# Optimization experiments

Hardware: AMD Instinct MI355X
Metric: run time of the kernel (lower is better)

Reference implementation:

```python
import jax, jax.numpy as jnp
import numpy as np

NX, NY = 8192, 8192
FX, FY = 1024, 1024
EMB, EMB_OUT = 512, 512


def setup_inputs() -> dict:
    key = jax.random.key(0)
    ks = jax.random.split(key, 8)
    s = lambda f: 1.0 / np.sqrt(f)
    return {
        "x": jax.random.normal(ks[0], (NX, FX), jnp.float32),
        "y": jax.random.normal(ks[1], (NY, FY), jnp.float32),
        "Wx": jax.random.uniform(ks[2], (FX, EMB), jnp.float32, -s(FX), s(FX)),
        "bx": jax.random.uniform(ks[3], (EMB,), jnp.float32, -s(FX), s(FX)),
        "Wy": jax.random.uniform(ks[4], (FY, EMB), jnp.float32, -s(FY), s(FY)),
        "by": jax.random.uniform(ks[5], (EMB,), jnp.float32, -s(FY), s(FY)),
        "Wg": jax.random.uniform(ks[6], (EMB, EMB_OUT), jnp.float32, -s(EMB), s(EMB)),
        "bg": jax.random.uniform(ks[7], (EMB_OUT,), jnp.float32, -s(EMB), s(EMB)),
    }


def reference(x, y, Wx, bx, Wy, by, Wg, bg):
    # Linear projections: [Nx, emb], [Ny, emb]
    xp = x @ Wx + bx
    yp = y @ Wy + by
    # Pairwise affinity (Dice-coefficient style normalization)
    A_ = xp @ yp.T                              # [Nx, Ny]
    Dcol = jnp.sum(xp * xp, axis=1)[:, None]    # ||x_i||^2, diag of xp@xp.T
    Drow = jnp.sum(yp * yp, axis=1)[None, :]    # ||y_j||^2, diag of yp@yp.T
    A = 2.0 * A_ / (Dcol + Drow)                # [Nx, Ny]
    # Weighted aggregation over x nodes, then ReLU MLP
    gwf = A.T @ xp                              # [Ny, emb]
    return jax.nn.relu(gwf @ Wg + bg)           # [Ny, emb_out]
```

## Files before the change

### kernel.cpp

```cpp
#include <hip/hip_runtime.h>
#include <hip/hip_bf16.h>


typedef __attribute__((ext_vector_type(8))) short bf16x8;
typedef __attribute__((ext_vector_type(4))) short bf16x4;
typedef __attribute__((ext_vector_type(4))) float f32x4;

__device__ __forceinline__ short f2b(float f) {
    unsigned int u = __builtin_bit_cast(unsigned int, f);
    unsigned int r = (u + 0x7fffu + ((u >> 16) & 1u)) >> 16;
    return (short)r;
}
__device__ __forceinline__ float b2f(short s) {
    unsigned int u = ((unsigned int)(unsigned short)s) << 16;
    return __builtin_bit_cast(float, u);
}

__device__ __forceinline__ void cp16(const void* g, void* l) {
    __builtin_amdgcn_global_load_lds(
        (const __attribute__((address_space(1))) void*)g,
        (__attribute__((address_space(3))) void*)l, 16, 0, 0);
}

constexpr int EPI_XP = 0;
constexpr int EPI_BF = 1;
constexpr int EPI_AT = 2;

template<int EPI, int TM, int TN>
__device__ __forceinline__ void gemm_core(
    const short* __restrict__ A, int lda,
    const short* __restrict__ Bt, int ldb,
    int N, int K, int bm, int bn, int kbase,
    const float* __restrict__ bias,
    short* __restrict__ outb,
    float* __restrict__ Dacc,
    const float* __restrict__ Drow, const float* __restrict__ Dcol)
{
    constexpr int FRM = (TN == 128) ? (TM / 32) : 2;
    __shared__ __align__(16) short As[TM * 32];
    __shared__ __align__(16) short Bs[TN * 32];

    const int tid  = threadIdx.x;
    const int wave = tid >> 6;
    const int lane = tid & 63;
    const int quad = lane >> 4;
    const int l15  = lane & 15;
    const int wn   = (TN == 128) ? (wave & 1) * 64 : 0;
    const int wm   = (TN == 128) ? (wave >> 1) * (FRM * 16) : wave * 32;

    f32x4 acc[FRM][4];
#pragma unroll
    for (int i = 0; i < FRM; i++)
#pragma unroll
        for (int j = 0; j < 4; j++) acc[i][j] = f32x4{0.f, 0.f, 0.f, 0.f};

    for (int k0 = kbase; k0 < kbase + K; k0 += 32) {
#pragma unroll
        for (int s = 0; s < TM / 64; s++) {
            const int seg = tid + 256 * s;
            const int row = seg >> 2, c8 = seg & 3;
            cp16(&A[(size_t)(bm + row) * lda + k0 + c8 * 8], &As[seg * 8]);
        }
#pragma unroll
        for (int s = 0; s < TN / 64; s++) {
            const int seg = tid + 256 * s;
            const int row = seg >> 2, c8 = seg & 3;
            cp16(&Bt[(size_t)(bn + row) * ldb + k0 + c8 * 8], &Bs[seg * 8]);
        }
        __syncthreads();

        bf16x8 a[FRM], b[4];
#pragma unroll
        for (int i = 0; i < FRM; i++)
            a[i] = *(const bf16x8*)&As[(wm + i * 16 + l15) * 32 + quad * 8];
#pragma unroll
        for (int j = 0; j < 4; j++)
            b[j] = *(const bf16x8*)&Bs[(wn + j * 16 + l15) * 32 + quad * 8];
#pragma unroll
        for (int i = 0; i < FRM; i++)
#pragma unroll
            for (int j = 0; j < 4; j++)
                acc[i][j] = __builtin_amdgcn_mfma_f32_16x16x32_bf16(a[i], b[j], acc[i][j], 0, 0, 0);
        __syncthreads();
    }

#pragma unroll
    for (int im = 0; im < FRM; ++im) {
#pragma unroll
        for (int r = 0; r < 4; ++r) {
            const int gm = bm + wm + im * 16 + quad * 4 + r;
            if (EPI == EPI_XP) {
                float s = 0.f;
#pragma unroll
                for (int jn = 0; jn < 4; ++jn) {
                    const int gn = bn + wn + jn * 16 + l15;
                    const float v = acc[im][jn][r] + bias[gn];
                    outb[(size_t)gm * N + gn] = f2b(v);
                    s += v * v;
                }
#pragma unroll
                for (int m = 1; m < 16; m <<= 1) s += __shfl_xor(s, m, 64);
                if (l15 == 0) atomicAdd(&Dacc[gm], s);
            } else if (EPI == EPI_BF) {
#pragma unroll
                for (int jn = 0; jn < 4; ++jn) {
                    const int gn = bn + wn + jn * 16 + l15;
                    outb[(size_t)gm * N + gn] = f2b(acc[im][jn][r]);
                }
            } else {
                const float dy = Drow[gm];
#pragma unroll
                for (int jn = 0; jn < 4; ++jn) {
                    const int gn = bn + wn + jn * 16 + l15;
                    const float v = 2.f * acc[im][jn][r] / (Dcol[gn] + dy);
                    outb[(size_t)gm * N + gn] = f2b(v);
                }
            }
        }
    }
}

__global__ __launch_bounds__(256)
void k_proj(const short* __restrict__ A, const short* __restrict__ Bt,
            const float* __restrict__ bias, short* __restrict__ outb,
            float* __restrict__ Dacc)
{
    gemm_core<EPI_XP, 64, 128>(A, 1024, Bt, 1024, 512, 1024,
                               blockIdx.y * 64, blockIdx.x * 128, 0,
                               bias, outb, Dacc, nullptr, nullptr);
}

__global__ __launch_bounds__(256)
void k_zT(const short* __restrict__ WgT, const short* __restrict__ xpb,
          short* __restrict__ zT)
{
    gemm_core<EPI_BF, 64, 128>(WgT, 512, xpb, 512, 8192, 512,
                               blockIdx.y * 64, blockIdx.x * 128, 0,
                               nullptr, zT, nullptr, nullptr, nullptr);
}

__global__ __launch_bounds__(256)
void k_aff(const short* __restrict__ ypb, const short* __restrict__ xpb,
           short* __restrict__ At, const float* __restrict__ Dy,
           const float* __restrict__ Dx)
{
    const int flat = blockIdx.x;
    const int x  = flat & 7;
    const int q  = flat >> 3;
    const int st = q >> 6;
    const int w  = q & 63;
    const int s  = x * 8 + st;
    const int bx = (s & 7) * 8 + (w & 7);
    const int by = (s >> 3) * 8 + (w >> 3);
    gemm_core<EPI_AT, 128, 128>(ypb, 512, xpb, 512, 8192, 512,
                                by * 128, bx * 128, 0,
                                nullptr, At, nullptr, Dy, Dx);
}

__global__ __launch_bounds__(256)
void k_agg(const short* __restrict__ At, const short* __restrict__ zT,
           short* __restrict__ p0, short* __restrict__ p1)
{
    const int flat = blockIdx.x;
    const int xcd = flat & 7;
    const int q   = flat >> 3;
    const int g   = xcd * 16 + (q >> 3);
    const int bm  = (g >> 1) * 128;
    const int z   = g & 1;
    const int bn  = (q & 7) * 64;
    short* outb = z ? p1 : p0;
    gemm_core<EPI_BF, 128, 64>(At, 8192, zT, 8192, 512, 4096,
                               bm, bn, z * 4096,
                               nullptr, outb, nullptr, nullptr, nullptr);
}

__global__ __launch_bounds__(256)
void k_fin(const short* __restrict__ p0, const short* __restrict__ p1,
           const float* __restrict__ bg, float* __restrict__ out)
{
    const int idx = (blockIdx.x * 256 + threadIdx.x) * 8;
    const int col = idx & 511;
    const bf16x8 a = *(const bf16x8*)&p0[idx];
    const bf16x8 b = *(const bf16x8*)&p1[idx];
    const f32x4 g0 = *(const f32x4*)&bg[col];
    const f32x4 g1 = *(const f32x4*)&bg[col + 4];
    f32x4 o0, o1;
#pragma unroll
    for (int e = 0; e < 4; ++e) {
        o0[e] = fmaxf(b2f(a[e]) + b2f(b[e]) + g0[e], 0.f);
        o1[e] = fmaxf(b2f(a[e + 4]) + b2f(b[e + 4]) + g1[e], 0.f);
    }
    *(f32x4*)&out[idx]     = o0;
    *(f32x4*)&out[idx + 4] = o1;
}

__global__ __launch_bounds__(256)
void k_cvt(const float* __restrict__ in, short* __restrict__ out)
{
    const int i = (blockIdx.x * 256 + threadIdx.x) * 4;
    const float4 v = *(const float4*)&in[i];
    bf16x4 b;
    b[0] = f2b(v.x); b[1] = f2b(v.y); b[2] = f2b(v.z); b[3] = f2b(v.w);
    *(bf16x4*)&out[i] = b;
}

__global__ __launch_bounds__(256)
void transpose_f32_bf16(const float* __restrict__ in, short* __restrict__ out, int R, int C)
{
    __shared__ short t[32][33];
    const int tx = threadIdx.x, ty = threadIdx.y;
    const int bx = blockIdx.x * 32, by = blockIdx.y * 32;
#pragma unroll
    for (int i = 0; i < 32; i += 8)
        t[ty + i][tx] = f2b(in[(size_t)(by + ty + i) * C + bx + tx]);
    __syncthreads();
#pragma unroll
    for (int i = 0; i < 32; i += 8)
        out[(size_t)(bx + ty + i) * R + by + tx] = t[tx][ty + i];
}

extern "C" void kernel_launch(void* const* d_in, const int* in_sizes, int n_in,
                              void* d_out, int out_size, void* d_ws, size_t ws_size,
                              hipStream_t stream)
{
    const float* x  = (const float*)d_in[0];
    const float* y  = (const float*)d_in[1];
    const float* Wx = (const float*)d_in[2];
    const float* bx = (const float*)d_in[3];
    const float* Wy = (const float*)d_in[4];
    const float* by = (const float*)d_in[5];
    const float* Wg = (const float*)d_in[6];
    const float* bg = (const float*)d_in[7];
    float* out = (float*)d_out;

    char* p = (char*)d_ws;
    short* At   = (short*)p;
    short* xb   = (short*)p;
    short* yb   = (short*)(p + (size_t)8192 * 1024 * 2);
    p += (size_t)8192 * 8192 * 2;
    short* xpb  = (short*)p; p += (size_t)8192 * 512 * 2;
    short* ypb  = (short*)p; p += (size_t)8192 * 512 * 2;
    short* zT   = (short*)p; p += (size_t)512 * 8192 * 2;
    short* WxT  = (short*)p; p += (size_t)512 * 1024 * 2;
    short* WyT  = (short*)p; p += (size_t)512 * 1024 * 2;
    short* WgT  = (short*)p; p += (size_t)512 * 512 * 2;
    float* Dx   = (float*)p; p += (size_t)8192 * 4;
    float* Dy   = (float*)p; p += (size_t)8192 * 4;
    short* p0 = xpb;
    short* p1 = ypb;

    hipMemsetAsync(Dx, 0, 2 * 8192 * sizeof(float), stream);

    dim3 tb(32, 8);
    transpose_f32_bf16<<<dim3(512 / 32, 1024 / 32), tb, 0, stream>>>(Wx, WxT, 1024, 512);
    transpose_f32_bf16<<<dim3(512 / 32, 1024 / 32), tb, 0, stream>>>(Wy, WyT, 1024, 512);
    transpose_f32_bf16<<<dim3(512 / 32, 512 / 32),  tb, 0, stream>>>(Wg, WgT, 512, 512);

    k_cvt<<<8192, 256, 0, stream>>>(x, xb);
    k_cvt<<<8192, 256, 0, stream>>>(y, yb);

    k_proj<<<dim3(4, 128), 256, 0, stream>>>(xb, WxT, bx, xpb, Dx);
    k_proj<<<dim3(4, 128), 256, 0, stream>>>(yb, WyT, by, ypb, Dy);

    k_zT<<<dim3(64, 8), 256, 0, stream>>>(WgT, xpb, zT);

    k_aff<<<4096, 256, 0, stream>>>(ypb, xpb, At, Dy, Dx);

    k_agg<<<1024, 256, 0, stream>>>(At, zT, p0, p1);

    k_fin<<<2048, 256, 0, stream>>>(p0, p1, bg, out);
}
```

Baseline: 379.8 us.

## Fuse fp32-to-bf16 input conversion into projection GEMM and widen affinity tiles

Removes the separate k_cvt passes over x and y by loading fp32 directly in the projection GEMM and converting to bf16 while staging into LDS. This drops a full write and re-read of the bf16 copies of the inputs. The affinity kernel switches to 128x256 tiles with a new XCD-aware block mapping and launch_bounds(256,2), and its normalization divide becomes a fast reciprocal multiply. The trade-off is that the projection A loads now go through registers instead of the async global-to-LDS path, and the larger affinity tiles raise register pressure.

```diff
diff --git a/kernel.cpp b/kernel.cpp
--- a/kernel.cpp
+++ b/kernel.cpp
@@ -26,9 +26,12 @@
 constexpr int EPI_BF = 1;
 constexpr int EPI_AT = 2;
 
-template<int EPI, int TM, int TN>
+constexpr int ASRC_BF16 = 0;
+constexpr int ASRC_F32  = 1;
+
+template<int EPI, int ASRC, int TM, int TN>
 __device__ __forceinline__ void gemm_core(
-    const short* __restrict__ A, int lda,
+    const void* __restrict__ Aptr, int lda,
     const short* __restrict__ Bt, int ldb,
     int N, int K, int bm, int bn, int kbase,
     const float* __restrict__ bias,
@@ -36,7 +39,10 @@
     float* __restrict__ Dacc,
     const float* __restrict__ Drow, const float* __restrict__ Dcol)
 {
-    constexpr int FRM = (TN == 128) ? (TM / 32) : 2;
+    constexpr int WN  = (TN >= 128) ? 2 : 1;
+    constexpr int WM  = 4 / WN;
+    constexpr int FRN = TN / WN / 16;
+    constexpr int FRM = TM / WM / 16;
     __shared__ __align__(16) short As[TM * 32];
     __shared__ __align__(16) short Bs[TN * 32];
 
@@ -45,21 +51,35 @@
     const int lane = tid & 63;
     const int quad = lane >> 4;
     const int l15  = lane & 15;
-    const int wn   = (TN == 128) ? (wave & 1) * 64 : 0;
-    const int wm   = (TN == 128) ? (wave >> 1) * (FRM * 16) : wave * 32;
-
-    f32x4 acc[FRM][4];
+    const int wn   = (wave % WN) * (FRN * 16);
+    const int wm   = (wave / WN) * (FRM * 16);
+
+    f32x4 acc[FRM][FRN];
 #pragma unroll
     for (int i = 0; i < FRM; i++)
 #pragma unroll
-        for (int j = 0; j < 4; j++) acc[i][j] = f32x4{0.f, 0.f, 0.f, 0.f};
+        for (int j = 0; j < FRN; j++) acc[i][j] = f32x4{0.f, 0.f, 0.f, 0.f};
 
     for (int k0 = kbase; k0 < kbase + K; k0 += 32) {
-#pragma unroll
-        for (int s = 0; s < TM / 64; s++) {
-            const int seg = tid + 256 * s;
-            const int row = seg >> 2, c8 = seg & 3;
-            cp16(&A[(size_t)(bm + row) * lda + k0 + c8 * 8], &As[seg * 8]);
+        if (ASRC == ASRC_F32) {
+            const float* Af = (const float*)Aptr;
+#pragma unroll
+            for (int s = 0; s < TM * 8 / 256; s++) {
+                const int seg = tid + 256 * s;
+                const int row = seg >> 3, c4 = seg & 7;
+                const float4 v = *(const float4*)&Af[(size_t)(bm + row) * lda + k0 + c4 * 4];
+                bf16x4 b;
+                b[0] = f2b(v.x); b[1] = f2b(v.y); b[2] = f2b(v.z); b[3] = f2b(v.w);
+                *(bf16x4*)&As[row * 32 + c4 * 4] = b;
+            }
+        } else {
+            const short* Ab = (const short*)Aptr;
+#pragma unroll
+            for (int s = 0; s < TM / 64; s++) {
+                const int seg = tid + 256 * s;
+                const int row = seg >> 2, c8 = seg & 3;
+                cp16(&Ab[(size_t)(bm + row) * lda + k0 + c8 * 8], &As[seg * 8]);
+            }
         }
 #pragma unroll
         for (int s = 0; s < TN / 64; s++) {
@@ -69,17 +89,17 @@
         }
         __syncthreads();
 
-        bf16x8 a[FRM], b[4];
+        bf16x8 a[FRM], b[FRN];
 #pragma unroll
         for (int i = 0; i < FRM; i++)
             a[i] = *(const bf16x8*)&As[(wm + i * 16 + l15) * 32 + quad * 8];
 #pragma unroll
-        for (int j = 0; j < 4; j++)
+        for (int j = 0; j < FRN; j++)
             b[j] = *(const bf16x8*)&Bs[(wn + j * 16 + l15) * 32 + quad * 8];
 #pragma unroll
         for (int i = 0; i < FRM; i++)
 #pragma unroll
-            for (int j = 0; j < 4; j++)
+            for (int j = 0; j < FRN; j++)
                 acc[i][j] = __builtin_amdgcn_mfma_f32_16x16x32_bf16(a[i], b[j], acc[i][j], 0, 0, 0);
         __syncthreads();
     }
@@ -92,7 +112,7 @@
             if (EPI == EPI_XP) {
                 float s = 0.f;
 #pragma unroll
-                for (int jn = 0; jn < 4; ++jn) {
+                for (int jn = 0; jn < FRN; ++jn) {
                     const int gn = bn + wn + jn * 16 + l15;
                     const float v = acc[im][jn][r] + bias[gn];
                     outb[(size_t)gm * N + gn] = f2b(v);
@@ -103,16 +123,16 @@
                 if (l15 == 0) atomicAdd(&Dacc[gm], s);
             } else if (EPI == EPI_BF) {
 #pragma unroll
-                for (int jn = 0; jn < 4; ++jn) {
+                for (int jn = 0; jn < FRN; ++jn) {
                     const int gn = bn + wn + jn * 16 + l15;
                     outb[(size_t)gm * N + gn] = f2b(acc[im][jn][r]);
                 }
             } else {
                 const float dy = Drow[gm];
 #pragma unroll
-                for (int jn = 0; jn < 4; ++jn) {
+                for (int jn = 0; jn < FRN; ++jn) {
                     const int gn = bn + wn + jn * 16 + l15;
-                    const float v = 2.f * acc[im][jn][r] / (Dcol[gn] + dy);
+                    const float v = 2.f * acc[im][jn][r] * __builtin_amdgcn_rcpf(Dcol[gn] + dy);
                     outb[(size_t)gm * N + gn] = f2b(v);
                 }
             }
@@ -121,40 +141,40 @@
 }
 
 __global__ __launch_bounds__(256)
-void k_proj(const short* __restrict__ A, const short* __restrict__ Bt,
+void k_proj(const float* __restrict__ A, const short* __restrict__ Bt,
             const float* __restrict__ bias, short* __restrict__ outb,
             float* __restrict__ Dacc)
 {
-    gemm_core<EPI_XP, 64, 128>(A, 1024, Bt, 1024, 512, 1024,
-                               blockIdx.y * 64, blockIdx.x * 128, 0,
-                               bias, outb, Dacc, nullptr, nullptr);
+    gemm_core<EPI_XP, ASRC_F32, 64, 128>(A, 1024, Bt, 1024, 512, 1024,
+                                         blockIdx.y * 64, blockIdx.x * 128, 0,
+                                         bias, outb, Dacc, nullptr, nullptr);
 }
 
 __global__ __launch_bounds__(256)
 void k_zT(const short* __restrict__ WgT, const short* __restrict__ xpb,
           short* __restrict__ zT)
 {
-    gemm_core<EPI_BF, 64, 128>(WgT, 512, xpb, 512, 8192, 512,
-                               blockIdx.y * 64, blockIdx.x * 128, 0,
-                               nullptr, zT, nullptr, nullptr, nullptr);
-}
-
-__global__ __launch_bounds__(256)
+    gemm_core<EPI_BF, ASRC_BF16, 64, 128>(WgT, 512, xpb, 512, 8192, 512,
+                                          blockIdx.y * 64, blockIdx.x * 128, 0,
+                                          nullptr, zT, nullptr, nullptr, nullptr);
+}
+
+__global__ __launch_bounds__(256, 2)
 void k_aff(const short* __restrict__ ypb, const short* __restrict__ xpb,
            short* __restrict__ At, const float* __restrict__ Dy,
            const float* __restrict__ Dx)
 {
     const int flat = blockIdx.x;
-    const int x  = flat & 7;
-    const int q  = flat >> 3;
-    const int st = q >> 6;
-    const int w  = q & 63;
-    const int s  = x * 8 + st;
-    const int bx = (s & 7) * 8 + (w & 7);
-    const int by = (s >> 3) * 8 + (w >> 3);
-    gemm_core<EPI_AT, 128, 128>(ypb, 512, xpb, 512, 8192, 512,
-                                by * 128, bx * 128, 0,
-                                nullptr, At, nullptr, Dy, Dx);
+    const int xcd = flat & 7;
+    const int q   = flat >> 3;
+    const int st  = q >> 5;
+    const int w   = q & 31;
+    const int s   = xcd * 8 + st;
+    const int bx  = (s & 7) * 4 + (w & 3);
+    const int by  = (s >> 3) * 8 + (w >> 2);
+    gemm_core<EPI_AT, ASRC_BF16, 128, 256>(ypb, 512, xpb, 512, 8192, 512,
+                                           by * 128, bx * 256, 0,
+                                           nullptr, At, nullptr, Dy, Dx);
 }
 
 __global__ __launch_bounds__(256)
@@ -169,9 +189,9 @@
     const int z   = g & 1;
     const int bn  = (q & 7) * 64;
     short* outb = z ? p1 : p0;
-    gemm_core<EPI_BF, 128, 64>(At, 8192, zT, 8192, 512, 4096,
-                               bm, bn, z * 4096,
-                               nullptr, outb, nullptr, nullptr, nullptr);
+    gemm_core<EPI_BF, ASRC_BF16, 128, 64>(At, 8192, zT, 8192, 512, 4096,
+                                          bm, bn, z * 4096,
+                                          nullptr, outb, nullptr, nullptr, nullptr);
 }
 
 __global__ __launch_bounds__(256)
@@ -192,16 +212,6 @@
     }
     *(f32x4*)&out[idx]     = o0;
     *(f32x4*)&out[idx + 4] = o1;
-}
-
-__global__ __launch_bounds__(256)
-void k_cvt(const float* __restrict__ in, short* __restrict__ out)
-{
-    const int i = (blockIdx.x * 256 + threadIdx.x) * 4;
-    const float4 v = *(const float4*)&in[i];
-    bf16x4 b;
-    b[0] = f2b(v.x); b[1] = f2b(v.y); b[2] = f2b(v.z); b[3] = f2b(v.w);
-    *(bf16x4*)&out[i] = b;
 }
 
 __global__ __launch_bounds__(256)
@@ -234,10 +244,7 @@
     float* out = (float*)d_out;
 
     char* p = (char*)d_ws;
-    short* At   = (short*)p;
-    short* xb   = (short*)p;
-    short* yb   = (short*)(p + (size_t)8192 * 1024 * 2);
-    p += (size_t)8192 * 8192 * 2;
+    short* At   = (short*)p; p += (size_t)8192 * 8192 * 2;
     short* xpb  = (short*)p; p += (size_t)8192 * 512 * 2;
     short* ypb  = (short*)p; p += (size_t)8192 * 512 * 2;
     short* zT   = (short*)p; p += (size_t)512 * 8192 * 2;
@@ -256,15 +263,12 @@
     transpose_f32_bf16<<<dim3(512 / 32, 1024 / 32), tb, 0, stream>>>(Wy, WyT, 1024, 512);
     transpose_f32_bf16<<<dim3(512 / 32, 512 / 32),  tb, 0, stream>>>(Wg, WgT, 512, 512);
 
-    k_cvt<<<8192, 256, 0, stream>>>(x, xb);
-    k_cvt<<<8192, 256, 0, stream>>>(y, yb);
-
-    k_proj<<<dim3(4, 128), 256, 0, stream>>>(xb, WxT, bx, xpb, Dx);
-    k_proj<<<dim3(4, 128), 256, 0, stream>>>(yb, WyT, by, ypb, Dy);
+    k_proj<<<dim3(4, 128), 256, 0, stream>>>(x, WxT, bx, xpb, Dx);
+    k_proj<<<dim3(4, 128), 256, 0, stream>>>(y, WyT, by, ypb, Dy);
 
     k_zT<<<dim3(64, 8), 256, 0, stream>>>(WgT, xpb, zT);
 
-    k_aff<<<4096, 256, 0, stream>>>(ypb, xpb, At, Dy, Dx);
+    k_aff<<<2048, 256, 0, stream>>>(ypb, xpb, At, Dy, Dx);
 
     k_agg<<<1024, 256, 0, stream>>>(At, zT, p0, p1);
 
```

Result: slower. 389.1 us (+2.5%).
